# Optimization experiments

Measured on AMD Instinct MI355X. Metric: run time of the kernel, lower is better.

The kernel has to match this reference:

```python
import jax, jax.numpy as jnp
import numpy as np

MAX_NODES = 32767   # complete binary tree, depth 15 (2**15 - 1)
N_FEATURES = 256
N_ACTIONS = 64
BATCH = 262144


def _build_tree(key):
    """Valid complete binary tree: internal node i has children 2i+1, 2i+2; leaves -1/-1."""
    idx = np.arange(MAX_NODES)
    left = 2 * idx + 1
    right = 2 * idx + 2
    internal = right < MAX_NODES
    children_left = np.where(internal, left, -1).astype(np.int32)
    children_right = np.where(internal, right, -1).astype(np.int32)
    k1, k2 = jax.random.split(key)
    features = jax.random.randint(k1, (MAX_NODES,), 0, N_FEATURES, dtype=jnp.int32)
    thresholds = jax.random.normal(k2, (MAX_NODES,), dtype=jnp.float32)
    return features, thresholds, jnp.asarray(children_left), jnp.asarray(children_right)


def setup_inputs() -> dict:
    key = jax.random.key(0)
    k_obs, k_tree, k_leaf = jax.random.split(key, 3)
    features, thresholds, children_left, children_right = _build_tree(k_tree)
    obs = jax.random.normal(k_obs, (BATCH, N_FEATURES), dtype=jnp.float32)
    leaf_logits = jax.random.normal(k_leaf, (MAX_NODES, N_ACTIONS), dtype=jnp.float32)
    return {
        "obs": obs,
        "features": features,
        "thresholds": thresholds,
        "children_left": children_left,
        "children_right": children_right,
        "leaf_logits": leaf_logits,
    }


def reference(obs, features, thresholds, children_left, children_right, leaf_logits):
    # Faithful translation of the flax module's while_loop tree traversal,
    # vmapped over a batch of observations.
    def traverse(o):  # o: [n_features]
        def cond(node_id):
            return children_left[node_id] != children_right[node_id]

        def body(node_id):
            go_left = o[features[node_id]] <= thresholds[node_id]
            return jax.lax.select(go_left, children_left[node_id], children_right[node_id])

        return jax.lax.while_loop(cond, body, jnp.int32(0))

    leaf_ids = jax.vmap(traverse)(obs)          # [B] int32
    return leaf_logits[leaf_ids]                # [B, n_actions]
```

## Files before the change

kernel.cpp:

```cpp
#include <hip/hip_runtime.h>


#define N_INTERN  16383
#define N_FEAT    256
#define N_ACT     64
#define BATCH     262144
#define BLOCK     256
#define GRID      256
#define ROWS_PB   (BATCH / GRID)
#define HROWS     32
#define HALVES    (ROWS_PB / HROWS)
#define DEPTH     14
#define PFN       8
#define HSLOTS    (HROWS * N_FEAT / 4)

typedef float f32x4 __attribute__((ext_vector_type(4)));

__global__ __launch_bounds__(BLOCK, 1) void tree_policy_kernel(
    const float* __restrict__ obs,
    const int*   __restrict__ features,
    const float* __restrict__ thresholds,
    const float* __restrict__ leaf_logits,
    float*       __restrict__ out)
{
    __shared__ float         sthr [N_INTERN];
    __shared__ unsigned char sfeat[N_INTERN];
    __shared__ __align__(16) float buf[2][HROWS * N_FEAT];

    const int tid  = threadIdx.x;
    const int lane = tid & 63;
    const long rowBase = (long)blockIdx.x * ROWS_PB;

    for (int i = tid; i < N_INTERN; i += BLOCK) {
        sthr[i]  = thresholds[i];
        sfeat[i] = (unsigned char)features[i];
    }

    const f32x4* gsrc = (const f32x4*)(obs + rowBase * N_FEAT);

    f32x4 pfA[PFN], pfB[PFN];
#pragma unroll
    for (int k = 0; k < PFN; ++k)
        pfA[k] = __builtin_nontemporal_load(&gsrc[0 * HSLOTS + k * BLOCK + tid]);
#pragma unroll
    for (int k = 0; k < PFN; ++k)
        pfB[k] = __builtin_nontemporal_load(&gsrc[1 * HSLOTS + k * BLOCK + tid]);

    asm volatile("s_waitcnt lgkmcnt(0)" ::: "memory");
    __builtin_amdgcn_s_barrier();

    const float thr_root  = sthr[0];
    const int   feat_root = sfeat[0];

    auto half_body = [&](int h, f32x4 (&pf)[PFN]) {
        const int b = h & 1;
        if (h == 0 || h == HALVES - 1)
            asm volatile("s_waitcnt vmcnt(8)" ::: "memory");
        else
            asm volatile("s_waitcnt vmcnt(12)" ::: "memory");
        __builtin_amdgcn_sched_barrier(0);
#pragma unroll
        for (int k = 0; k < PFN; ++k)
            *(f32x4*)&buf[b][(k * BLOCK + tid) * 4] = pf[k];
        if (h + 2 < HALVES) {
#pragma unroll
            for (int k = 0; k < PFN; ++k)
                pf[k] = __builtin_nontemporal_load(&gsrc[(h + 2) * HSLOTS + k * BLOCK + tid]);
        }
        asm volatile("s_waitcnt lgkmcnt(0)" ::: "memory");
        __builtin_amdgcn_s_barrier();
        __builtin_amdgcn_sched_barrier(0);

        const float* myrow = &buf[b][(lane & 31) * N_FEAT];
        int   node = 0;
        float tcur = thr_root;
        int   fcur = feat_root;
#pragma unroll
        for (int d = 0; d < DEPTH - 1; ++d) {
            const float x   = myrow[fcur];
            const int   c   = 2 * node + 1;
            const float tl  = sthr[c];
            const float trr = sthr[c + 1];
            const int   fl  = sfeat[c];
            const int   fr  = sfeat[c + 1];
            const bool  L   = (x <= tcur);
            node = L ? c : c + 1;
            tcur = L ? tl : trr;
            fcur = L ? fl : fr;
        }
        {
            const float x = myrow[fcur];
            node = 2 * node + ((x <= tcur) ? 1 : 2);
        }

        const long outRow0 = rowBase + (long)h * HROWS;
#pragma unroll
        for (int j = 0; j < 2; ++j) {
            const int fid   = j * BLOCK + tid;
            const int r     = fid >> 4;
            const int chunk = fid & 15;
            const int leaf  = __shfl(node, r, 64);
            const f32x4 v   = *(const f32x4*)(leaf_logits + (size_t)leaf * N_ACT + chunk * 4);
            __builtin_nontemporal_store(v, (f32x4*)(out + (outRow0 + r) * N_ACT + chunk * 4));
        }
    };

    for (int h = 0; h < HALVES; h += 2) {
        half_body(h,     pfA);
        half_body(h + 1, pfB);
    }
}

extern "C" void kernel_launch(void* const* d_in, const int* in_sizes, int n_in,
                              void* d_out, int out_size, void* d_ws, size_t ws_size,
                              hipStream_t stream) {
    const float* obs         = (const float*)d_in[0];
    const int*   features    = (const int*)  d_in[1];
    const float* thresholds  = (const float*)d_in[2];
    const float* leaf_logits = (const float*)d_in[5];
    float*       out         = (float*)d_out;

    tree_policy_kernel<<<dim3(GRID), dim3(BLOCK), 0, stream>>>(
        obs, features, thresholds, leaf_logits, out);
}
```

Before: 67.24 us.

## Swizzle shared obs rows to avoid bank conflicts and pack child thresholds

Observation rows staged in shared memory are now stored with a per-row rotation of 16-byte slots and a per-wave element rotation. Lanes reading random features from different rows then land in different banks. Tree node data is repacked as sibling pairs (float2 thresholds, packed byte features), so each level does one threshold load and one feature load instead of four dependent LDS reads. The cost is extra index arithmetic on the critical traversal chain and four branchy store variants.

Result: slower. 70.68 us (+5.1%).

```diff
diff --git a/kernel.cpp b/kernel.cpp
--- a/kernel.cpp
+++ b/kernel.cpp
@@ -1,7 +1,7 @@
 #include <hip/hip_runtime.h>
 
 
-#define N_INTERN  16383
+#define N_PAIR    8191
 #define N_FEAT    256
 #define N_ACT     64
 #define BATCH     262144
@@ -12,9 +12,26 @@
 #define HALVES    (ROWS_PB / HROWS)
 #define DEPTH     14
 #define PFN       8
-#define HSLOTS    (HROWS * N_FEAT / 4)
+#define TSLOTS    (HROWS * N_FEAT / 4)
 
 typedef float f32x4 __attribute__((ext_vector_type(4)));
+
+template<int ROT>
+__device__ __forceinline__ void store_rot(f32x4* dst, const f32x4 (&pf)[PFN], int tid) {
+#pragma unroll
+    for (int k = 0; k < PFN; ++k) {
+        const int s = k * BLOCK + tid;
+        const int r = s >> 6;
+        const int c = s & 63;
+        const f32x4 v = pf[k];
+        f32x4 w;
+        w.x = v[(0 - ROT) & 3];
+        w.y = v[(1 - ROT) & 3];
+        w.z = v[(2 - ROT) & 3];
+        w.w = v[(3 - ROT) & 3];
+        dst[r * 64 + ((c + (r >> 2)) & 63)] = w;
+    }
+}
 
 __global__ __launch_bounds__(BLOCK, 1) void tree_policy_kernel(
     const float* __restrict__ obs,
@@ -23,34 +40,37 @@
     const float* __restrict__ leaf_logits,
     float*       __restrict__ out)
 {
-    __shared__ float         sthr [N_INTERN];
-    __shared__ unsigned char sfeat[N_INTERN];
-    __shared__ __align__(16) float buf[2][HROWS * N_FEAT];
+    __shared__ float2         sthr2 [N_PAIR];
+    __shared__ unsigned short sfeat2[N_PAIR];
+    __shared__ __align__(16) f32x4 buf[2][TSLOTS];
 
     const int tid  = threadIdx.x;
     const int lane = tid & 63;
     const long rowBase = (long)blockIdx.x * ROWS_PB;
+    const f32x4* gsrc = (const f32x4*)(obs + rowBase * N_FEAT);
 
-    for (int i = tid; i < N_INTERN; i += BLOCK) {
-        sthr[i]  = thresholds[i];
-        sfeat[i] = (unsigned char)features[i];
+    for (int i = tid; i < N_PAIR; i += BLOCK) {
+        sthr2[i]  = make_float2(thresholds[2 * i + 1], thresholds[2 * i + 2]);
+        sfeat2[i] = (unsigned short)((features[2 * i + 1] & 255) |
+                                     ((features[2 * i + 2] & 255) << 8));
     }
-
-    const f32x4* gsrc = (const f32x4*)(obs + rowBase * N_FEAT);
+    const float thr_root  = thresholds[0];
+    const int   feat_root = features[0];
 
     f32x4 pfA[PFN], pfB[PFN];
 #pragma unroll
     for (int k = 0; k < PFN; ++k)
-        pfA[k] = __builtin_nontemporal_load(&gsrc[0 * HSLOTS + k * BLOCK + tid]);
+        pfA[k] = __builtin_nontemporal_load(&gsrc[0 * TSLOTS + k * BLOCK + tid]);
 #pragma unroll
     for (int k = 0; k < PFN; ++k)
-        pfB[k] = __builtin_nontemporal_load(&gsrc[1 * HSLOTS + k * BLOCK + tid]);
+        pfB[k] = __builtin_nontemporal_load(&gsrc[1 * TSLOTS + k * BLOCK + tid]);
 
     asm volatile("s_waitcnt lgkmcnt(0)" ::: "memory");
     __builtin_amdgcn_s_barrier();
 
-    const float thr_root  = sthr[0];
-    const int   feat_root = sfeat[0];
+    const int r    = lane & 31;
+    const int rq   = r >> 2;
+    const int rbase = r * 256;
 
     auto half_body = [&](int h, f32x4 (&pf)[PFN]) {
         const int b = h & 1;
@@ -59,37 +79,38 @@
         else
             asm volatile("s_waitcnt vmcnt(12)" ::: "memory");
         __builtin_amdgcn_sched_barrier(0);
-#pragma unroll
-        for (int k = 0; k < PFN; ++k)
-            *(f32x4*)&buf[b][(k * BLOCK + tid) * 4] = pf[k];
+        switch (tid >> 6) {
+            case 0: store_rot<0>(&buf[b][0], pf, tid); break;
+            case 1: store_rot<1>(&buf[b][0], pf, tid); break;
+            case 2: store_rot<2>(&buf[b][0], pf, tid); break;
+            default: store_rot<3>(&buf[b][0], pf, tid); break;
+        }
         if (h + 2 < HALVES) {
 #pragma unroll
             for (int k = 0; k < PFN; ++k)
-                pf[k] = __builtin_nontemporal_load(&gsrc[(h + 2) * HSLOTS + k * BLOCK + tid]);
+                pf[k] = __builtin_nontemporal_load(
+                    &gsrc[(long)(h + 2) * TSLOTS + k * BLOCK + tid]);
         }
         asm volatile("s_waitcnt lgkmcnt(0)" ::: "memory");
         __builtin_amdgcn_s_barrier();
         __builtin_amdgcn_sched_barrier(0);
 
-        const float* myrow = &buf[b][(lane & 31) * N_FEAT];
+        const float* bufc = (const float*)&buf[b][0];
         int   node = 0;
         float tcur = thr_root;
         int   fcur = feat_root;
 #pragma unroll
         for (int d = 0; d < DEPTH - 1; ++d) {
-            const float x   = myrow[fcur];
-            const int   c   = 2 * node + 1;
-            const float tl  = sthr[c];
-            const float trr = sthr[c + 1];
-            const int   fl  = sfeat[c];
-            const int   fr  = sfeat[c + 1];
-            const bool  L   = (x <= tcur);
-            node = L ? c : c + 1;
-            tcur = L ? tl : trr;
-            fcur = L ? fl : fr;
+            const float x = bufc[rbase + ((((fcur >> 2) + rq) & 63) << 2) + ((fcur + r) & 3)];
+            const float2   tch = sthr2[node];
+            const unsigned fp  = sfeat2[node];
+            const bool L = (x <= tcur);
+            node = 2 * node + (L ? 1 : 2);
+            tcur = L ? tch.x : tch.y;
+            fcur = (int)(L ? (fp & 255u) : (fp >> 8));
         }
         {
-            const float x = myrow[fcur];
+            const float x = bufc[rbase + ((((fcur >> 2) + rq) & 63) << 2) + ((fcur + r) & 3)];
             node = 2 * node + ((x <= tcur) ? 1 : 2);
         }
 
@@ -97,17 +118,17 @@
 #pragma unroll
         for (int j = 0; j < 2; ++j) {
             const int fid   = j * BLOCK + tid;
-            const int r     = fid >> 4;
+            const int rr    = fid >> 4;
             const int chunk = fid & 15;
-            const int leaf  = __shfl(node, r, 64);
+            const int leaf  = __shfl(node, rr, 64);
             const f32x4 v   = *(const f32x4*)(leaf_logits + (size_t)leaf * N_ACT + chunk * 4);
-            __builtin_nontemporal_store(v, (f32x4*)(out + (outRow0 + r) * N_ACT + chunk * 4));
+            __builtin_nontemporal_store(v, (f32x4*)(out + (outRow0 + rr) * N_ACT + chunk * 4));
         }
     };
 
-    for (int h = 0; h < HALVES; h += 2) {
-        half_body(h,     pfA);
-        half_body(h + 1, pfB);
+    for (int hh = 0; hh < HALVES; hh += 2) {
+        half_body(hh,     pfA);
+        half_body(hh + 1, pfB);
     }
 }
 
```
